# Optimization experiments

Hardware: AMD Instinct MI355X
Metric: run time of the kernel (lower is better)

The kernel has to match this reference:

```python
import jax, jax.numpy as jnp
import numpy as np

T, B, I, HID = 512, 64, 512, 1024


def setup_inputs() -> dict:
    key = jax.random.key(0)
    k1, k2, k3, k4, k5 = jax.random.split(key, 5)
    scale = 1.0 / np.sqrt(I + HID)
    return {
        "x": jax.random.normal(k1, (T, B, I), dtype=jnp.float32),
        "Wz": jax.random.normal(k2, (HID, I + HID), dtype=jnp.float32) * scale,
        "bz": jax.random.normal(k3, (HID,), dtype=jnp.float32) * scale,
        "Wh": jax.random.normal(k4, (HID, I + HID), dtype=jnp.float32) * scale,
        "bh": jax.random.normal(k5, (HID,), dtype=jnp.float32) * scale,
    }


def reference(x, Wz, bz, Wh, bh):
    # x: [T, B, I]; Wz/Wh: [HID, HID+I] (applied to cat([h, x], axis=1))
    t, b, _ = x.shape
    hid = Wz.shape[0]

    def step(h, xt):
        inp = jnp.concatenate([h, xt], axis=1)          # [B, HID+I]
        g = jax.nn.sigmoid(inp @ Wz.T + bz)             # linear_z
        z = g
        r = g  # faithful to source: r also uses linear_z (linear_r unused)
        cand = jnp.tanh(jnp.concatenate([r * h, xt], axis=1) @ Wh.T + bh)
        h_new = (1.0 - z) * h + z * cand
        return h_new, (h_new, z, r)

    h0 = jnp.zeros((b, hid), dtype=x.dtype)
    _, (Hs, Z, R) = jax.lax.scan(step, h0, x)
    H = jnp.concatenate([h0[None], Hs], axis=0)          # [T+1, B, HID]
    return H, Z, R
```

## Files before the change

kernel.cpp:

```cpp
#include <hip/hip_runtime.h>
#include <cstdint>

typedef unsigned short ushort_t;
typedef __attribute__((ext_vector_type(8))) short short8;
typedef __attribute__((ext_vector_type(4))) float f32x4;
typedef unsigned long long u64;

#define T_STEPS 512
#define BATCH   64
#define IDIM    512
#define HIDDEN  1024
#define NWGP    256
#define BH      (BATCH*HIDDEN)
#define STG     65536
#define SCRR    73728
#define SCRT    77824

__device__ __forceinline__ ushort_t f2bf(float f) {
  unsigned int x = __float_as_uint(f);
  unsigned int r = (x + 0x7fffu + ((x >> 16) & 1u)) >> 16;
  return (ushort_t)r;
}
__device__ __forceinline__ float sigmoid_f(float x) { return 1.f / (1.f + __expf(-x)); }
__device__ __forceinline__ float tanh_f(float x)    { return 1.f - 2.f / (1.f + __expf(2.f * x)); }

#define WAITV(N) asm volatile("s_waitcnt vmcnt(" #N ")" ::: "memory")

__device__ __forceinline__ void glds16(const ushort_t* g, ushort_t* l) {
  __builtin_amdgcn_global_load_lds(
      (const __attribute__((address_space(1))) void*)g,
      (__attribute__((address_space(3))) void*)l, 16, 0, 17);
}

#define STAGE4(SRC) do { \
  glds16((SRC),       &smem[stgw]); \
  glds16((SRC) + 64,  &smem[stgw + 512]); \
  glds16((SRC) + 128, &smem[stgw + 1024]); \
  glds16((SRC) + 192, &smem[stgw + 1536]); \
} while (0)

#define KSTEPG(J, VN, WOFF) do { \
  const int k0_ = kqbase + (J) * 32 + koff; \
  short8 b0_ = *(const short8*)&smem[(WOFF) + wb0 + (k0_ ^ sz0)]; \
  short8 b1_ = *(const short8*)&smem[(WOFF) + wb1 + (k0_ ^ sz1)]; \
  WAITV(VN); \
  __builtin_amdgcn_sched_barrier(0); \
  short8 a_ = *(const short8*)&smem[abase + ((J) >> 1) * 512 + (axq ^ (((J) & 1) * 32))]; \
  acc0 = __builtin_amdgcn_mfma_f32_16x16x32_bf16(a_, b0_, acc0, 0, 0, 0); \
  acc1 = __builtin_amdgcn_mfma_f32_16x16x32_bf16(a_, b1_, acc1, 0, 0, 0); \
} while (0)

#define MATVEC8G(WOFF) do { \
  KSTEPG(0,3,WOFF); KSTEPG(1,3,WOFF); KSTEPG(2,2,WOFF); KSTEPG(3,2,WOFF); \
  KSTEPG(4,1,WOFF); KSTEPG(5,1,WOFF); KSTEPG(6,0,WOFF); KSTEPG(7,0,WOFF); \
} while (0)

#define POLL_GRP(TGT) do { \
  if (tid == 0) { \
    while (__hip_atomic_load(gctr, __ATOMIC_RELAXED, __HIP_MEMORY_SCOPE_AGENT) < (TGT)) \
      __builtin_amdgcn_s_sleep(1); \
  } \
  __syncthreads(); \
  WAITV(0); \
  __builtin_amdgcn_sched_barrier(0); \
} while (0)

__global__ __launch_bounds__(256) void convert_weights(
    const float* __restrict__ Wz, const float* __restrict__ Wh,
    ushort_t* __restrict__ Wzh, ushort_t* __restrict__ Wzx,
    ushort_t* __restrict__ Whh, ushort_t* __restrict__ Whx)
{
  int j = blockIdx.x;
  const float* W = blockIdx.y ? Wh : Wz;
  ushort_t* Bh = blockIdx.y ? Whh : Wzh;
  ushort_t* Bx = blockIdx.y ? Whx : Wzx;
  const float* row = W + (size_t)j * (HIDDEN + IDIM);
  for (int c = threadIdx.x; c < HIDDEN + IDIM; c += 256) {
    ushort_t v = f2bf(row[c]);
    if (c < HIDDEN) Bh[(size_t)j * HIDDEN + c] = v;
    else            Bx[(size_t)j * IDIM + (c - HIDDEN)] = v;
  }
}

__global__ __launch_bounds__(256) void gx_gemm(
    const float* __restrict__ x,
    const ushort_t* __restrict__ Wzx, const ushort_t* __restrict__ Whx,
    const float* __restrict__ bz, const float* __restrict__ bh,
    float* __restrict__ outZ, float* __restrict__ outR)
{
  const int which = blockIdx.z;
  const ushort_t* W = which ? Whx : Wzx;
  const float* bias = which ? bh : bz;
  float* out = which ? outR : outZ;
  const int m0 = blockIdx.x * 64;
  const int n0 = blockIdx.y * 64;
  __shared__ ushort_t As[64 * 40];
  __shared__ ushort_t Bs[64 * 40];
  const int tid = threadIdx.x;
  const int lane = tid & 63, w4 = tid >> 6;
  const int row = tid >> 2, q = tid & 3;
  f32x4 acc[4] = {{0,0,0,0},{0,0,0,0},{0,0,0,0},{0,0,0,0}};
  for (int kk = 0; kk < IDIM; kk += 32) {
    const float* xs = &x[(size_t)(m0 + row) * IDIM + kk + q * 8];
    float4 f0 = *(const float4*)xs;
    float4 f1 = *(const float4*)(xs + 4);
    short8 av;
    av[0]=f2bf(f0.x); av[1]=f2bf(f0.y); av[2]=f2bf(f0.z); av[3]=f2bf(f0.w);
    av[4]=f2bf(f1.x); av[5]=f2bf(f1.y); av[6]=f2bf(f1.z); av[7]=f2bf(f1.w);
    short8 bv = *(const short8*)&W[(size_t)(n0 + row) * IDIM + kk + q * 8];
    __syncthreads();
    *(short8*)&As[row * 40 + q * 8] = av;
    *(short8*)&Bs[row * 40 + q * 8] = bv;
    __syncthreads();
    short8 af = *(const short8*)&As[(w4 * 16 + (lane & 15)) * 40 + (lane >> 4) * 8];
    #pragma unroll
    for (int c = 0; c < 4; ++c) {
      short8 bf = *(const short8*)&Bs[(c * 16 + (lane & 15)) * 40 + (lane >> 4) * 8];
      acc[c] = __builtin_amdgcn_mfma_f32_16x16x32_bf16(af, bf, acc[c], 0, 0, 0);
    }
  }
  #pragma unroll
  for (int c = 0; c < 4; ++c) {
    int j = n0 + c * 16 + (lane & 15);
    float bv = bias[j];
    #pragma unroll
    for (int r = 0; r < 4; ++r) {
      int m = m0 + w4 * 16 + (lane >> 4) * 4 + r;
      out[(size_t)m * HIDDEN + j] = acc[c][r] + bv;
    }
  }
}

__global__ __launch_bounds__(256) void gru_persist(
    const ushort_t* __restrict__ Wzh, const ushort_t* __restrict__ Whh,
    float* __restrict__ H, float* __restrict__ Z, float* __restrict__ R,
    u64* __restrict__ h_buf, u64* __restrict__ ghb, int* __restrict__ ctrs)
{
  extern __shared__ ushort_t smem[];
  const int tid = threadIdx.x;
  const int lane = tid & 63, wv = tid >> 6;
  const int grp = blockIdx.x & 7, slot = blockIdx.x >> 3;
  const int rbase = grp * 8;
  const int jbase = slot * 32;
  int* gctr = ctrs + grp * 32;
  const ushort_t* hgu = (const ushort_t*)h_buf;
  const ushort_t* ggu = (const ushort_t*)ghb;

  for (int c = tid; c < 32 * 128; c += 256) {
    int row = c >> 7, k8 = (c & 127) * 8;
    int dst = row * 1024 + (k8 ^ ((row & 7) << 3));
    *(short8*)&smem[dst]         = *(const short8*)&Wzh[(size_t)(jbase + row) * 1024 + k8];
    *(short8*)&smem[32768 + dst] = *(const short8*)&Whh[(size_t)(jbase + row) * 1024 + k8];
  }
  __syncthreads();

  if (tid < 64) {
    float4 z4 = {0.f, 0.f, 0.f, 0.f};
    *(float4*)&H[(size_t)(rbase + (tid >> 3)) * 1024 + jbase + (tid & 7) * 4] = z4;
  }

  const int li = lane & 15, q4 = lane >> 4;
  const int kqbase = wv * 256;
  const int koff = q4 * 8;
  const int wb0 = li * 1024,     wb1 = (16 + li) * 1024;
  const int sz0 = (li & 7) << 3, sz1 = ((16 + li) & 7) << 3;
  const int m0 = q4 * 4;
  const int col = jbase + (wv & 1) * 16 + li;
  const int srow = lane >> 3, schk = (lane & 7) ^ srow;
  const ushort_t* srcAh = hgu + (size_t)(rbase + srow) * 1024 + kqbase + schk * 8;
  const ushort_t* srcAg = ggu + (size_t)(rbase + srow) * 1024 + kqbase + schk * 8;
  const int stgw = STG + wv * 2048;
  const int abase = stgw + (li & 7) * 64;
  const int axq = (q4 ^ (li & 7)) * 8;
  const int bidx = (rbase + (tid >> 3)) * 256 + slot * 8 + (tid & 7);
  const int scrt_rd = SCRT + (tid >> 3) * 40 + (tid & 7) * 4;
  const int rr0 = SCRR + ((0 * 4 + wv) * 64 + lane) * 8;
  const int rr1 = SCRR + ((1 * 4 + wv) * 64 + lane) * 8;
  const int rrc = SCRR + ((wv & 1) * 4 * 64 + lane) * 8;

  float hreg[4] = {0.f, 0.f, 0.f, 0.f};
  float g[4], hn[4], gz[4], gh[4];

  for (int t = 0; t < T_STEPS; ++t) {
    const size_t zoff = (size_t)t * BH;

    if (wv < 2 && q4 < 2)
      #pragma unroll
      for (int r = 0; r < 4; ++r) {
        gz[r] = Z[zoff + (size_t)(rbase + m0 + r) * 1024 + col];
        gh[r] = R[zoff + (size_t)(rbase + m0 + r) * 1024 + col];
      }

    POLL_GRP(64 * t);

    f32x4 acc0 = {0, 0, 0, 0}, acc1 = {0, 0, 0, 0};
    STAGE4(srcAh);
    MATVEC8G(0);

    *(f32x4*)&smem[rr0] = acc0;
    *(f32x4*)&smem[rr1] = acc1;
    __syncthreads();
    if (wv < 2) {
      f32x4 s = *(const f32x4*)&smem[rrc];
      #pragma unroll
      for (int q = 1; q < 4; ++q) {
        f32x4 o = *(const f32x4*)&smem[rrc + q * 64 * 8];
        #pragma unroll
        for (int r = 0; r < 4; ++r) s[r] += o[r];
      }
      #pragma unroll
      for (int r = 0; r < 4; ++r) g[r] = sigmoid_f(s[r] + gz[r]);
      if (q4 < 2)
        #pragma unroll
        for (int r = 0; r < 4; ++r)
          smem[SCRT + (m0 + r) * 40 + (wv & 1) * 16 + li] = f2bf(g[r] * hreg[r]);
    }
    __syncthreads();
    if (tid < 64) {
      u64 v = *(const u64*)&smem[scrt_rd];
      __hip_atomic_store(ghb + bidx, v, __ATOMIC_RELAXED, __HIP_MEMORY_SCOPE_AGENT);
    }
    WAITV(0);
    __syncthreads();
    if (tid == 0)
      __hip_atomic_fetch_add(gctr, 1, __ATOMIC_RELAXED, __HIP_MEMORY_SCOPE_AGENT);

    POLL_GRP(64 * t + 32);

    acc0 = (f32x4){0, 0, 0, 0}; acc1 = (f32x4){0, 0, 0, 0};
    STAGE4(srcAg);
    MATVEC8G(32768);

    *(f32x4*)&smem[rr0] = acc0;
    *(f32x4*)&smem[rr1] = acc1;
    __syncthreads();
    if (wv < 2) {
      f32x4 s = *(const f32x4*)&smem[rrc];
      #pragma unroll
      for (int q = 1; q < 4; ++q) {
        f32x4 o = *(const f32x4*)&smem[rrc + q * 64 * 8];
        #pragma unroll
        for (int r = 0; r < 4; ++r) s[r] += o[r];
      }
      #pragma unroll
      for (int r = 0; r < 4; ++r) {
        float cand = tanh_f(s[r] + gh[r]);
        hn[r] = (1.f - g[r]) * hreg[r] + g[r] * cand;
        hreg[r] = hn[r];
      }
      if (q4 < 2)
        #pragma unroll
        for (int r = 0; r < 4; ++r)
          smem[SCRT + (m0 + r) * 40 + (wv & 1) * 16 + li] = f2bf(hn[r]);
    }
    __syncthreads();
    if (tid < 64) {
      u64 v = *(const u64*)&smem[scrt_rd];
      __hip_atomic_store(h_buf + bidx, v, __ATOMIC_RELAXED, __HIP_MEMORY_SCOPE_AGENT);
    }
    WAITV(0);
    __syncthreads();
    if (tid == 0)
      __hip_atomic_fetch_add(gctr, 1, __ATOMIC_RELAXED, __HIP_MEMORY_SCOPE_AGENT);

    if (wv < 2 && q4 < 2) {
      const size_t hoff = (size_t)(t + 1) * BH;
      #pragma unroll
      for (int r = 0; r < 4; ++r) {
        const size_t rowo = (size_t)(rbase + m0 + r) * 1024 + col;
        Z[zoff + rowo] = g[r];
        R[zoff + rowo] = g[r];
        H[hoff + rowo] = hn[r];
      }
    }
  }
}

extern "C" void kernel_launch(void* const* d_in, const int* in_sizes, int n_in,
                              void* d_out, int out_size, void* d_ws, size_t ws_size,
                              hipStream_t stream) {
  (void)in_sizes; (void)n_in; (void)out_size; (void)ws_size;
  const float* x  = (const float*)d_in[0];
  const float* Wz = (const float*)d_in[1];
  const float* bz = (const float*)d_in[2];
  const float* Wh = (const float*)d_in[3];
  const float* bh = (const float*)d_in[4];

  float* H = (float*)d_out;
  float* Z = H + (size_t)(T_STEPS + 1) * BH;
  float* R = Z + (size_t)T_STEPS * BH;

  char* ws = (char*)d_ws;
  int*      ctrs  = (int*)ws;
  u64*      h_buf = (u64*)(ws + 16384);
  u64*      ghb   = (u64*)(ws + 16384 + 131072);
  ushort_t* Wzh   = (ushort_t*)(ws + 16384 + 2 * 131072);
  ushort_t* Whh   = Wzh + (size_t)HIDDEN * HIDDEN;
  ushort_t* Wzx   = Whh + (size_t)HIDDEN * HIDDEN;
  ushort_t* Whx   = Wzx + (size_t)HIDDEN * IDIM;

  hipFuncSetAttribute((const void*)gru_persist,
                      hipFuncAttributeMaxDynamicSharedMemorySize, 156416);

  hipMemsetAsync(ctrs, 0, 16384, stream);
  hipMemsetAsync(h_buf, 0, 131072, stream);
  convert_weights<<<dim3(HIDDEN, 2), 256, 0, stream>>>(Wz, Wh, Wzh, Wzx, Whh, Whx);
  gx_gemm<<<dim3(T_STEPS * BATCH / 64, HIDDEN / 64, 2), 256, 0, stream>>>(
      x, Wzx, Whx, bz, bh, Z, R);
  gru_persist<<<NWGP, 256, 156416, stream>>>(Wzh, Whh, H, Z, R, h_buf, ghb, ctrs);
}
```

Baseline: 2.401 ms.

## Transpose MFMA operands to write packed hidden state directly and fuse input GEMMs

Swaps the A/B operands of the recurrent MFMA so each lane holds four consecutive hidden columns of one batch row. The epilogue can then pack four bf16 values into one u64 and store straight to the global exchange buffers, removing the shared-memory scratch transpose and one barrier per phase. Z/R/H loads and stores become float4. The input projection GEMM is also fused to compute both gates from one staged x tile, so x is converted once instead of twice. It risks breaking the row/column mapping of the exchange layout if the transposed indexing is wrong.

```diff
diff --git a/kernel.cpp b/kernel.cpp
--- a/kernel.cpp
+++ b/kernel.cpp
@@ -14,7 +14,6 @@
 #define BH      (BATCH*HIDDEN)
 #define STG     65536
 #define SCRR    73728
-#define SCRT    77824
 
 __device__ __forceinline__ ushort_t f2bf(float f) {
   unsigned int x = __float_as_uint(f);
@@ -46,8 +45,8 @@
   WAITV(VN); \
   __builtin_amdgcn_sched_barrier(0); \
   short8 a_ = *(const short8*)&smem[abase + ((J) >> 1) * 512 + (axq ^ (((J) & 1) * 32))]; \
-  acc0 = __builtin_amdgcn_mfma_f32_16x16x32_bf16(a_, b0_, acc0, 0, 0, 0); \
-  acc1 = __builtin_amdgcn_mfma_f32_16x16x32_bf16(a_, b1_, acc1, 0, 0, 0); \
+  acc0 = __builtin_amdgcn_mfma_f32_16x16x32_bf16(b0_, a_, acc0, 0, 0, 0); \
+  acc1 = __builtin_amdgcn_mfma_f32_16x16x32_bf16(b1_, a_, acc1, 0, 0, 0); \
 } while (0)
 
 #define MATVEC8G(WOFF) do { \
@@ -82,24 +81,22 @@
   }
 }
 
-__global__ __launch_bounds__(256) void gx_gemm(
+__global__ __launch_bounds__(256) void gx_gemm2(
     const float* __restrict__ x,
     const ushort_t* __restrict__ Wzx, const ushort_t* __restrict__ Whx,
     const float* __restrict__ bz, const float* __restrict__ bh,
     float* __restrict__ outZ, float* __restrict__ outR)
 {
-  const int which = blockIdx.z;
-  const ushort_t* W = which ? Whx : Wzx;
-  const float* bias = which ? bh : bz;
-  float* out = which ? outR : outZ;
   const int m0 = blockIdx.x * 64;
   const int n0 = blockIdx.y * 64;
   __shared__ ushort_t As[64 * 40];
-  __shared__ ushort_t Bs[64 * 40];
+  __shared__ ushort_t Bzs[64 * 40];
+  __shared__ ushort_t Bhs[64 * 40];
   const int tid = threadIdx.x;
   const int lane = tid & 63, w4 = tid >> 6;
   const int row = tid >> 2, q = tid & 3;
-  f32x4 acc[4] = {{0,0,0,0},{0,0,0,0},{0,0,0,0},{0,0,0,0}};
+  f32x4 accz[4] = {{0,0,0,0},{0,0,0,0},{0,0,0,0},{0,0,0,0}};
+  f32x4 acch[4] = {{0,0,0,0},{0,0,0,0},{0,0,0,0},{0,0,0,0}};
   for (int kk = 0; kk < IDIM; kk += 32) {
     const float* xs = &x[(size_t)(m0 + row) * IDIM + kk + q * 8];
     float4 f0 = *(const float4*)xs;
@@ -107,26 +104,31 @@
     short8 av;
     av[0]=f2bf(f0.x); av[1]=f2bf(f0.y); av[2]=f2bf(f0.z); av[3]=f2bf(f0.w);
     av[4]=f2bf(f1.x); av[5]=f2bf(f1.y); av[6]=f2bf(f1.z); av[7]=f2bf(f1.w);
-    short8 bv = *(const short8*)&W[(size_t)(n0 + row) * IDIM + kk + q * 8];
-    __syncthreads();
-    *(short8*)&As[row * 40 + q * 8] = av;
-    *(short8*)&Bs[row * 40 + q * 8] = bv;
+    short8 bzv = *(const short8*)&Wzx[(size_t)(n0 + row) * IDIM + kk + q * 8];
+    short8 bhv = *(const short8*)&Whx[(size_t)(n0 + row) * IDIM + kk + q * 8];
+    __syncthreads();
+    *(short8*)&As[row * 40 + q * 8]  = av;
+    *(short8*)&Bzs[row * 40 + q * 8] = bzv;
+    *(short8*)&Bhs[row * 40 + q * 8] = bhv;
     __syncthreads();
     short8 af = *(const short8*)&As[(w4 * 16 + (lane & 15)) * 40 + (lane >> 4) * 8];
     #pragma unroll
     for (int c = 0; c < 4; ++c) {
-      short8 bf = *(const short8*)&Bs[(c * 16 + (lane & 15)) * 40 + (lane >> 4) * 8];
-      acc[c] = __builtin_amdgcn_mfma_f32_16x16x32_bf16(af, bf, acc[c], 0, 0, 0);
+      short8 bzf = *(const short8*)&Bzs[(c * 16 + (lane & 15)) * 40 + (lane >> 4) * 8];
+      short8 bhf = *(const short8*)&Bhs[(c * 16 + (lane & 15)) * 40 + (lane >> 4) * 8];
+      accz[c] = __builtin_amdgcn_mfma_f32_16x16x32_bf16(af, bzf, accz[c], 0, 0, 0);
+      acch[c] = __builtin_amdgcn_mfma_f32_16x16x32_bf16(af, bhf, acch[c], 0, 0, 0);
     }
   }
   #pragma unroll
   for (int c = 0; c < 4; ++c) {
     int j = n0 + c * 16 + (lane & 15);
-    float bv = bias[j];
+    float bzv = bz[j], bhv = bh[j];
     #pragma unroll
     for (int r = 0; r < 4; ++r) {
       int m = m0 + w4 * 16 + (lane >> 4) * 4 + r;
-      out[(size_t)m * HIDDEN + j] = acc[c][r] + bv;
+      outZ[(size_t)m * HIDDEN + j] = accz[c][r] + bzv;
+      outR[(size_t)m * HIDDEN + j] = acch[c][r] + bhv;
     }
   }
 }
@@ -164,16 +166,16 @@
   const int koff = q4 * 8;
   const int wb0 = li * 1024,     wb1 = (16 + li) * 1024;
   const int sz0 = (li & 7) << 3, sz1 = ((16 + li) & 7) << 3;
-  const int m0 = q4 * 4;
-  const int col = jbase + (wv & 1) * 16 + li;
   const int srow = lane >> 3, schk = (lane & 7) ^ srow;
   const ushort_t* srcAh = hgu + (size_t)(rbase + srow) * 1024 + kqbase + schk * 8;
   const ushort_t* srcAg = ggu + (size_t)(rbase + srow) * 1024 + kqbase + schk * 8;
   const int stgw = STG + wv * 2048;
   const int abase = stgw + (li & 7) * 64;
   const int axq = (q4 ^ (li & 7)) * 8;
-  const int bidx = (rbase + (tid >> 3)) * 256 + slot * 8 + (tid & 7);
-  const int scrt_rd = SCRT + (tid >> 3) * 40 + (tid & 7) * 4;
+  const bool epi = (wv < 2) && (li < 8);
+  const int erow = rbase + li;
+  const int ecol = jbase + (wv & 1) * 16 + q4 * 4;
+  const int gidx = (erow * 1024 + ecol) >> 2;
   const int rr0 = SCRR + ((0 * 4 + wv) * 64 + lane) * 8;
   const int rr1 = SCRR + ((1 * 4 + wv) * 64 + lane) * 8;
   const int rrc = SCRR + ((wv & 1) * 4 * 64 + lane) * 8;
@@ -184,12 +186,12 @@
   for (int t = 0; t < T_STEPS; ++t) {
     const size_t zoff = (size_t)t * BH;
 
-    if (wv < 2 && q4 < 2)
-      #pragma unroll
-      for (int r = 0; r < 4; ++r) {
-        gz[r] = Z[zoff + (size_t)(rbase + m0 + r) * 1024 + col];
-        gh[r] = R[zoff + (size_t)(rbase + m0 + r) * 1024 + col];
-      }
+    if (epi) {
+      f32x4 z4 = *(const f32x4*)&Z[zoff + (size_t)erow * 1024 + ecol];
+      f32x4 r4 = *(const f32x4*)&R[zoff + (size_t)erow * 1024 + ecol];
+      #pragma unroll
+      for (int r = 0; r < 4; ++r) { gz[r] = z4[r]; gh[r] = r4[r]; }
+    }
 
     POLL_GRP(64 * t);
 
@@ -200,7 +202,7 @@
     *(f32x4*)&smem[rr0] = acc0;
     *(f32x4*)&smem[rr1] = acc1;
     __syncthreads();
-    if (wv < 2) {
+    if (epi) {
       f32x4 s = *(const f32x4*)&smem[rrc];
       #pragma unroll
       for (int q = 1; q < 4; ++q) {
@@ -210,15 +212,11 @@
       }
       #pragma unroll
       for (int r = 0; r < 4; ++r) g[r] = sigmoid_f(s[r] + gz[r]);
-      if (q4 < 2)
-        #pragma unroll
-        for (int r = 0; r < 4; ++r)
-          smem[SCRT + (m0 + r) * 40 + (wv & 1) * 16 + li] = f2bf(g[r] * hreg[r]);
-    }
-    __syncthreads();
-    if (tid < 64) {
-      u64 v = *(const u64*)&smem[scrt_rd];
-      __hip_atomic_store(ghb + bidx, v, __ATOMIC_RELAXED, __HIP_MEMORY_SCOPE_AGENT);
+      u64 v = (u64)f2bf(g[0] * hreg[0])
+            | ((u64)f2bf(g[1] * hreg[1]) << 16)
+            | ((u64)f2bf(g[2] * hreg[2]) << 32)
+            | ((u64)f2bf(g[3] * hreg[3]) << 48);
+      __hip_atomic_store(ghb + gidx, v, __ATOMIC_RELAXED, __HIP_MEMORY_SCOPE_AGENT);
     }
     WAITV(0);
     __syncthreads();
@@ -234,7 +232,7 @@
     *(f32x4*)&smem[rr0] = acc0;
     *(f32x4*)&smem[rr1] = acc1;
     __syncthreads();
-    if (wv < 2) {
+    if (epi) {
       f32x4 s = *(const f32x4*)&smem[rrc];
       #pragma unroll
       for (int q = 1; q < 4; ++q) {
@@ -248,30 +246,25 @@
         hn[r] = (1.f - g[r]) * hreg[r] + g[r] * cand;
         hreg[r] = hn[r];
       }
-      if (q4 < 2)
-        #pragma unroll
-        for (int r = 0; r < 4; ++r)
-          smem[SCRT + (m0 + r) * 40 + (wv & 1) * 16 + li] = f2bf(hn[r]);
-    }
-    __syncthreads();
-    if (tid < 64) {
-      u64 v = *(const u64*)&smem[scrt_rd];
-      __hip_atomic_store(h_buf + bidx, v, __ATOMIC_RELAXED, __HIP_MEMORY_SCOPE_AGENT);
+      u64 v = (u64)f2bf(hn[0])
+            | ((u64)f2bf(hn[1]) << 16)
+            | ((u64)f2bf(hn[2]) << 32)
+            | ((u64)f2bf(hn[3]) << 48);
+      __hip_atomic_store(h_buf + gidx, v, __ATOMIC_RELAXED, __HIP_MEMORY_SCOPE_AGENT);
     }
     WAITV(0);
     __syncthreads();
     if (tid == 0)
       __hip_atomic_fetch_add(gctr, 1, __ATOMIC_RELAXED, __HIP_MEMORY_SCOPE_AGENT);
 
-    if (wv < 2 && q4 < 2) {
+    if (epi) {
       const size_t hoff = (size_t)(t + 1) * BH;
-      #pragma unroll
-      for (int r = 0; r < 4; ++r) {
-        const size_t rowo = (size_t)(rbase + m0 + r) * 1024 + col;
-        Z[zoff + rowo] = g[r];
-        R[zoff + rowo] = g[r];
-        H[hoff + rowo] = hn[r];
-      }
+      const size_t rowo = (size_t)erow * 1024 + ecol;
+      float4 gv = {g[0], g[1], g[2], g[3]};
+      float4 hv = {hn[0], hn[1], hn[2], hn[3]};
+      *(float4*)&Z[zoff + rowo] = gv;
+      *(float4*)&R[zoff + rowo] = gv;
+      *(float4*)&H[hoff + rowo] = hv;
     }
   }
 }
@@ -300,12 +293,12 @@
   ushort_t* Whx   = Wzx + (size_t)HIDDEN * IDIM;
 
   hipFuncSetAttribute((const void*)gru_persist,
-                      hipFuncAttributeMaxDynamicSharedMemorySize, 156416);
+                      hipFuncAttributeMaxDynamicSharedMemorySize, 155648);
 
   hipMemsetAsync(ctrs, 0, 16384, stream);
   hipMemsetAsync(h_buf, 0, 131072, stream);
   convert_weights<<<dim3(HIDDEN, 2), 256, 0, stream>>>(Wz, Wh, Wzh, Wzx, Whh, Whx);
-  gx_gemm<<<dim3(T_STEPS * BATCH / 64, HIDDEN / 64, 2), 256, 0, stream>>>(
+  gx_gemm2<<<dim3(T_STEPS * BATCH / 64, HIDDEN / 64), 256, 0, stream>>>(
       x, Wzx, Whx, bz, bh, Z, R);
-  gru_persist<<<NWGP, 256, 156416, stream>>>(Wzh, Whh, H, Z, R, h_buf, ghb, ctrs);
-}
+  gru_persist<<<NWGP, 256, 155648, stream>>>(Wzh, Whh, H, Z, R, h_buf, ghb, ctrs);
+}
```

After: 2.346 ms. 1.02x faster.
